# Kernel optimization log

Hardware: AMD Instinct MI355X
Metric: run time of the kernel (lower is better)

The kernel has to match this reference:

```python
import jax, jax.numpy as jnp
import numpy as np

N_QUBITS = 12
DIM = 2 ** N_QUBITS
N_RES_LAYERS = 3
N_HEADS = 2
N_ATTN_LAYERS = 2
SEQ_LEN = 64
HORIZON = 4
BATCH = 8
N_PARAMS = N_QUBITS * 2 * N_ATTN_LAYERS  # 48
FEAT = N_QUBITS * N_HEADS  # 24

# ---- static (numpy) precomputed gate structures (little-endian, qiskit convention) ----
_idx = np.arange(DIM)

def _cx_perm(c, t):
    # CNOT: flip target bit where control bit is 1 -> index permutation
    return np.where(((_idx >> c) & 1) == 1, _idx ^ (1 << t), _idx)

def _cz_phase(a, b):
    return (1.0 - 2.0 * (((_idx >> a) & 1) * ((_idx >> b) & 1))).astype(np.float32)

CX_LADDER = [jnp.asarray(_cx_perm(i, i + 1)) for i in range(N_QUBITS - 1)]
CX_RING = jnp.asarray(_cx_perm(N_QUBITS - 1, 0))
CX_LONG = jnp.asarray(_cx_perm(0, N_QUBITS - 1))
_CZ = []
for _layer in range(N_RES_LAYERS):
    _ph = np.ones(DIM, np.float32)
    for _i in range(_layer % 2, N_QUBITS - 1, 2):
        _ph *= _cz_phase(_i, _i + 1)
    _CZ.append(jnp.asarray(_ph))
# Qiskit Pauli label 'I'*i + 'Z' + 'I'*(n-i-1) acts on qubit n-1-i (big-endian labels)
Z_SIGNS = jnp.asarray(np.stack([
    (1.0 - 2.0 * ((_idx >> (N_QUBITS - 1 - i)) & 1)).astype(np.float32)
    for i in range(N_QUBITS)]))  # (n, DIM)


def _apply_1q(state, gate, q):
    # state: (..., DIM); gate: (2,2) or (...,2,2) broadcastable against leading dims
    hi = DIM >> (q + 1)
    lo = 1 << q
    s = state.reshape(state.shape[:-1] + (hi, 2, lo))
    out = jnp.einsum('...ij,...hjl->...hil', gate, s)
    return out.reshape(state.shape)


def _ry(theta):
    c = jnp.cos(theta / 2)
    s = jnp.sin(theta / 2)
    g = jnp.stack([jnp.stack([c, -s], -1), jnp.stack([s, c], -1)], -2)
    return g.astype(jnp.complex64)


def _rz(phi):
    em = jnp.exp(-0.5j * phi)
    ep = jnp.exp(0.5j * phi)
    z = jnp.zeros_like(em)
    return jnp.stack([jnp.stack([em, z], -1), jnp.stack([z, ep], -1)], -2)


def _u3(t, p, l):
    ct = jnp.cos(t / 2).astype(jnp.complex64)
    st = jnp.sin(t / 2).astype(jnp.complex64)
    return jnp.stack([jnp.stack([ct, -jnp.exp(1j * l) * st]),
                      jnp.stack([jnp.exp(1j * p) * st, jnp.exp(1j * (p + l)) * ct])])


def _encode_reservoir(x, res_params):
    # x: (B,T) normalized scalars -> batched statevectors (B,T,DIM)
    B, T = x.shape
    # H^{\otimes n} |0...0> = uniform superposition
    state = jnp.full((B, T, DIM), 1.0 / np.sqrt(DIM), jnp.complex64)
    for i in range(N_QUBITS):
        state = _apply_1q(state, _ry(x * np.pi * (i + 1) / N_QUBITS), i)
        state = _apply_1q(state, _rz(x * np.pi / (i + 1)), i)
    for p in CX_LADDER:
        state = state[..., p]
    state = state[..., CX_RING]
    # fixed random reservoir
    for layer in range(N_RES_LAYERS):
        for i in range(N_QUBITS):
            g = _u3(res_params[layer, i, 0], res_params[layer, i, 1], res_params[layer, i, 2])
            state = _apply_1q(state, g, i)
        state = state * _CZ[layer]
        state = state[..., CX_LONG]  # n > 2
    return state


def _project(state, params):
    # projection circuit: per layer RY/RZ on each qubit then CNOT ladder; then <Z_i>
    for layer in range(N_ATTN_LAYERS):
        for i in range(N_QUBITS):
            k = (layer * N_QUBITS + i) * 2
            state = _apply_1q(state, _ry(params[k]), i)
            state = _apply_1q(state, _rz(params[k + 1]), i)
        for p in CX_LADDER:
            state = state[..., p]
    probs = state.real ** 2 + state.imag ** 2  # (B,T,DIM)
    return jnp.einsum('btd,qd->btq', probs, Z_SIGNS)  # (B,T,n)


def setup_inputs() -> dict:
    key = jax.random.key(0)
    ks = jax.random.split(key, 6)
    sequence = jax.random.uniform(ks[0], (BATCH, SEQ_LEN), jnp.float32)
    res_params = jax.random.uniform(ks[1], (N_RES_LAYERS, N_QUBITS, 3), jnp.float32,
                                    minval=0.0, maxval=2.0 * np.pi)
    head_params = jax.random.uniform(ks[2], (N_HEADS, 3, N_PARAMS), jnp.float32,
                                     minval=0.0, maxval=2.0 * np.pi)
    W1 = jax.random.normal(ks[3], (FEAT, 2 * FEAT), jnp.float32) / np.sqrt(FEAT)
    b1 = jnp.zeros((2 * FEAT,), jnp.float32)
    W2 = jax.random.normal(ks[4], (2 * FEAT, HORIZON), jnp.float32) / np.sqrt(2 * FEAT)
    b2 = jnp.zeros((HORIZON,), jnp.float32)
    return {'sequence': sequence, 'res_params': res_params, 'head_params': head_params,
            'W1': W1, 'b1': b1, 'W2': W2, 'b2': b2}


def reference(sequence, res_params, head_params, W1, b1, W2, b2):
    states = _encode_reservoir(sequence, res_params)  # (B,T,DIM)
    T = sequence.shape[1]
    mask = jnp.triu(jnp.full((T, T), -1e9, jnp.float32), k=1)
    outs = []
    for h in range(N_HEADS):
        Q = _project(states, head_params[h, 0])
        K = _project(states, head_params[h, 1])
        V = _project(states, head_params[h, 2])
        scores = jnp.einsum('btd,bsd->bts', Q, K) / np.sqrt(N_QUBITS) + mask
        attn = jax.nn.softmax(scores, axis=-1)
        outs.append(jnp.einsum('bts,bsd->btd', attn, V))
    feats = jnp.concatenate(outs, -1)  # (B,T,FEAT)
    last = feats[:, -1, :]
    hdn = jax.nn.gelu(last @ W1 + b1, approximate=False)  # torch GELU default = exact erf
    pred = hdn @ W2 + b2  # (B, HORIZON)
    return pred
```

## Files before the change

### kernel.cpp

```cpp
#include <hip/hip_runtime.h>
#include <hip/hip_bf16.h>


#define PADDED 4224

__device__ __forceinline__ int PD(int j) { return j + (j >> 5); }

__device__ __forceinline__ int mapIdx(int j, int mode) {
  if (mode == 1) { int k = j ^ ((j >> 11) & 1); return k ^ ((k & 0x7FF) << 1); }
  if (mode == 2) { return j ^ ((j & 1) << 11); }
  if (mode == 3) { return j ^ ((j & 0x7FF) << 1); }
  return j;
}

template <int L>
__device__ __forceinline__ int layoutIdx(int tid, int r) {
  if constexpr (L == 0) return (tid << 4) | r;
  else if constexpr (L == 1) return ((tid & 0xF0) << 4) | (r << 4) | (tid & 15);
  else return (r << 8) | tid;
}

template <int L>
__device__ __forceinline__ void ldsRead16(const float* sR, const float* sI, int tid, int mode,
                                          float ar[16], float ai[16]) {
#pragma unroll
  for (int r = 0; r < 16; ++r) {
    int j = layoutIdx<L>(tid, r);
    int a = PD(mapIdx(j, mode));
    ar[r] = sR[a]; ai[r] = sI[a];
  }
}

template <int L>
__device__ __forceinline__ void ldsWrite16(float* sR, float* sI, int tid,
                                           const float ar[16], const float ai[16], int czmask) {
#pragma unroll
  for (int r = 0; r < 16; ++r) {
    int j = layoutIdx<L>(tid, r);
    float vr = ar[r], vi = ai[r];
    if (czmask) {
      float sg = (__popc((j & (j >> 1)) & czmask) & 1) ? -1.0f : 1.0f;
      vr *= sg; vi *= sg;
    }
    int a = PD(j);
    sR[a] = vr; sI[a] = vi;
  }
}

__device__ __forceinline__ void applyU34(float ar[16], float ai[16], const float (*ut)[8]) {
#pragma unroll
  for (int b = 0; b < 4; ++b) {
    const float* u = ut[b];
    float u00r = u[0];
    float u01r = u[2], u01i = u[3];
    float u10r = u[4], u10i = u[5], u11r = u[6], u11i = u[7];
#pragma unroll
    for (int m = 0; m < 8; ++m) {
      int p0 = ((m >> b) << (b + 1)) | (m & ((1 << b) - 1));
      int p1 = p0 | (1 << b);
      float x0r = ar[p0], x0i = ai[p0], x1r = ar[p1], x1i = ai[p1];
      ar[p0] = u00r * x0r + u01r * x1r - u01i * x1i;
      ai[p0] = u00r * x0i + u01r * x1i + u01i * x1r;
      ar[p1] = u10r * x0r - u10i * x0i + u11r * x1r - u11i * x1i;
      ai[p1] = u10r * x0i + u10i * x0r + u11r * x1i + u11i * x1r;
    }
  }
}

__device__ __forceinline__ void applyRyRz4(float ar[16], float ai[16], const float4* gt) {
#pragma unroll
  for (int b = 0; b < 4; ++b) {
    float4 g = gt[b];
    float c = g.x, s = g.y, zr = g.z, zi = g.w;
#pragma unroll
    for (int m = 0; m < 8; ++m) {
      int p0 = ((m >> b) << (b + 1)) | (m & ((1 << b) - 1));
      int p1 = p0 | (1 << b);
      float x0r = ar[p0], x0i = ai[p0], x1r = ar[p1], x1i = ai[p1];
      float n0r = c * x0r - s * x1r;
      float n0i = c * x0i - s * x1i;
      float wr  = s * x0r + c * x1r;
      float wi  = s * x0i + c * x1i;
      ar[p0] = n0r;              ai[p0] = n0i;
      ar[p1] = wr * zr - wi * zi; ai[p1] = wr * zi + wi * zr;
    }
  }
}

template <int L>
__device__ __forceinline__ void encPass(float* sR, float* sI, int tid, int mode,
                                        const float (*ut)[8], int czmask) {
  float ar[16], ai[16];
  ldsRead16<L>(sR, sI, tid, mode, ar, ai);
  if (mode != 0) __syncthreads();
  applyU34(ar, ai, ut);
  ldsWrite16<L>(sR, sI, tid, ar, ai, czmask);
  __syncthreads();
}

template <int L>
__device__ __forceinline__ void projPass(float* sR, float* sI, int tid, int mode, const float4* gt) {
  float ar[16], ai[16];
  ldsRead16<L>(sR, sI, tid, mode, ar, ai);
  if (mode != 0) __syncthreads();
  applyRyRz4(ar, ai, gt);
  ldsWrite16<L>(sR, sI, tid, ar, ai, 0);
  __syncthreads();
}

__device__ __forceinline__ void projFinal(const float* sR, const float* sI, int tid,
                                          const float4* gt, float feat[12]) {
  float ar[16], ai[16];
#pragma unroll
  for (int r = 0; r < 16; ++r) {
    int a = PD((r << 8) | tid);
    ar[r] = sR[a]; ai[r] = sI[a];
  }
  applyRyRz4(ar, ai, gt);
  float sp = 0.f, f0 = 0.f, f1 = 0.f, f2 = 0.f, f3 = 0.f;
  int pt = __popc(tid) & 1;
#pragma unroll
  for (int r = 0; r < 16; ++r) {
    float p = ar[r] * ar[r] + ai[r] * ai[r];
    sp += p;
    int tr = r ^ (r << 1); tr ^= (tr << 2);
    f0 += ((pt ^ ((tr >> 3) & 1)) ? -p : p);
    f1 += ((pt ^ ((tr >> 2) & 1)) ? -p : p);
    f2 += ((pt ^ ((tr >> 1) & 1)) ? -p : p);
    f3 += ((pt ^ (tr & 1)) ? -p : p);
  }
  feat[0] = f0; feat[1] = f1; feat[2] = f2; feat[3] = f3;
  int tt = tid ^ (tid << 1); tt ^= (tt << 2); tt ^= (tt << 4);
#pragma unroll
  for (int q = 4; q < 12; ++q)
    feat[q] = ((tt >> (11 - q)) & 1) ? -sp : sp;
}

__device__ __forceinline__ float waveReduce(float v) {
#pragma unroll
  for (int off = 32; off; off >>= 1) v += __shfl_xor(v, off, 64);
  return v;
}


__device__ __forceinline__ void buildQtab(float4* qtab, int tid, float x) {
  const float PI = 3.14159265358979323846f;
  const float RS2 = 0.70710678118654752440f;
  if (tid < 12) {
    int i = tid;
    float th = x * PI * (float)(i + 1) / 12.0f;
    float ph = x * PI / (float)(i + 1);
    float s, c;  sincosf(0.5f * th, &s, &c);
    float zi, zr; sincosf(0.5f * ph, &zi, &zr);
    float k0 = (c - s) * RS2, k1 = (c + s) * RS2;
    qtab[i] = make_float4(k0 * zr, -k0 * zi, k1 * zr, k1 * zi);
  }
}

__device__ __forceinline__ void buildUtab(float (*utab)[8], int tid, const float* resp) {
  if (tid >= 64 && tid < 100) {
    int i = tid - 64;
    const float* rp = resp + i * 3;
    float st, ct;  sincosf(0.5f * rp[0], &st, &ct);
    float sp2, cp; sincosf(rp[1], &sp2, &cp);
    float sl, cl;  sincosf(rp[2], &sl, &cl);
    float spl, cpl; sincosf(rp[1] + rp[2], &spl, &cpl);
    float* u = utab[i];
    u[0] = ct;       u[1] = 0.0f;
    u[2] = -cl * st; u[3] = -sl * st;
    u[4] = cp * st;  u[5] = sp2 * st;
    u[6] = cpl * ct; u[7] = spl * ct;
  }
}

__device__ __forceinline__ void initProduct(float* sRe, float* sIm, int tid, const float4* qtab) {
  float pr, pi;
  {
    float4 g = qtab[4];
    int sb = tid & 1;
    pr = sb ? g.z : g.x; pi = sb ? g.w : g.y;
  }
#pragma unroll
  for (int q = 5; q < 12; ++q) {
    float4 g = qtab[q];
    int sb = (tid >> (q - 4)) & 1;
    float fr = sb ? g.z : g.x, fi = sb ? g.w : g.y;
    float nr = pr * fr - pi * fi;
    pi = pr * fi + pi * fr; pr = nr;
  }
  float4 g0 = qtab[0], g1 = qtab[1], g2 = qtab[2], g3 = qtab[3];
  float c01r[4], c01i[4], c23r[4], c23i[4];
#pragma unroll
  for (int i2 = 0; i2 < 4; ++i2) {
    float f0r = (i2 & 1) ? g0.z : g0.x, f0i = (i2 & 1) ? g0.w : g0.y;
    float f1r = (i2 & 2) ? g1.z : g1.x, f1i = (i2 & 2) ? g1.w : g1.y;
    c01r[i2] = f0r * f1r - f0i * f1i; c01i[i2] = f0r * f1i + f0i * f1r;
    float f2r = (i2 & 1) ? g2.z : g2.x, f2i = (i2 & 1) ? g2.w : g2.y;
    float f3r = (i2 & 2) ? g3.z : g3.x, f3i = (i2 & 2) ? g3.w : g3.y;
    c23r[i2] = f2r * f3r - f2i * f3i; c23i[i2] = f2r * f3i + f2i * f3r;
  }
#pragma unroll
  for (int r = 0; r < 16; ++r) {
    float lr = c01r[r & 3] * c23r[r >> 2] - c01i[r & 3] * c23i[r >> 2];
    float li = c01r[r & 3] * c23i[r >> 2] + c01i[r & 3] * c23r[r >> 2];
    int a = PD((tid << 4) | r);
    sRe[a] = pr * lr - pi * li;
    sIm[a] = pr * li + pi * lr;
  }
}

__device__ __forceinline__ void buildPtab(float4* ptab, int tid, const float* hp) {
  if (tid < 24) {
    int k = tid * 2;
    float s, c;  sincosf(0.5f * hp[k], &s, &c);
    float zi, zr; sincosf(hp[k + 1], &zi, &zr);
    ptab[tid] = make_float4(c, s, zr, zi);
  }
}


__global__ __launch_bounds__(256, 2) void enc_kernel(
    const float* __restrict__ seq, const float* __restrict__ resp,
    float* __restrict__ wsStates) {
  __shared__ float sRe[PADDED], sIm[PADDED];
  __shared__ float4 qtab[12];
  __shared__ float utab[36][8];

  const int tid = threadIdx.x;
  const int blk = blockIdx.x;
  const float x = seq[blk];

  buildQtab(qtab, tid, x);
  buildUtab(utab, tid, resp);
  __syncthreads();

  initProduct(sRe, sIm, tid, qtab);
  __syncthreads();

  encPass<0>(sRe, sIm, tid, 1, &utab[0], 0);
  encPass<1>(sRe, sIm, tid, 0, &utab[4], 0);
  encPass<2>(sRe, sIm, tid, 0, &utab[8], 0x555);
  encPass<0>(sRe, sIm, tid, 2, &utab[12], 0);
  encPass<1>(sRe, sIm, tid, 0, &utab[16], 0);
  encPass<2>(sRe, sIm, tid, 0, &utab[20], 0x2AA);
  encPass<0>(sRe, sIm, tid, 2, &utab[24], 0);
  encPass<1>(sRe, sIm, tid, 0, &utab[28], 0);

  {
    float ar[16], ai[16];
    ldsRead16<2>(sRe, sIm, tid, 0, ar, ai);
    applyU34(ar, ai, &utab[32]);
    float* gR = wsStates + (size_t)blk * 8192;
    float* gI = gR + 4096;
#pragma unroll
    for (int r = 0; r < 16; ++r) {
      int j = (r << 8) | tid;
      float sg = (__popc((j & (j >> 1)) & 0x555) & 1) ? -1.0f : 1.0f;
      int g = j ^ ((j & 1) << 11);
      gR[g] = sg * ar[r];
      gI[g] = sg * ai[r];
    }
  }
}

__global__ __launch_bounds__(256, 4) void proj_kernel(
    const float* __restrict__ wsStates, const float* __restrict__ hparams,
    float* __restrict__ featBase) {
  __shared__ float sRe[PADDED], sIm[PADDED];
  __shared__ float4 ptab[24];
  __shared__ float red[4][12];

  const int tid = threadIdx.x;
  const int bid = blockIdx.x;
  int h, which, s;
  if (bid < 2048) { s = bid >> 2; int pp = bid & 3; h = pp >> 1; which = 1 + (pp & 1); }
  else            { int i = bid - 2048; h = i & 1; s = (((i >> 1) << 6) | 63); which = 0; }
  const int b = s >> 6, t = s & 63;

  buildPtab(ptab, tid, hparams + (h * 3 + which) * 48);

  float ar[16], ai[16];
  const float4* pR = (const float4*)(wsStates + (size_t)s * 8192 + (tid << 4));
  const float4* pI = (const float4*)(wsStates + (size_t)s * 8192 + 4096 + (tid << 4));
#pragma unroll
  for (int k = 0; k < 4; ++k) {
    float4 vr = pR[k], vi = pI[k];
    ar[4 * k] = vr.x; ar[4 * k + 1] = vr.y; ar[4 * k + 2] = vr.z; ar[4 * k + 3] = vr.w;
    ai[4 * k] = vi.x; ai[4 * k + 1] = vi.y; ai[4 * k + 2] = vi.z; ai[4 * k + 3] = vi.w;
  }
  __syncthreads();

  applyRyRz4(ar, ai, &ptab[0]);
  ldsWrite16<0>(sRe, sIm, tid, ar, ai, 0);
  __syncthreads();

  projPass<1>(sRe, sIm, tid, 0, &ptab[4]);
  projPass<2>(sRe, sIm, tid, 0, &ptab[8]);
  projPass<0>(sRe, sIm, tid, 3, &ptab[12]);
  projPass<1>(sRe, sIm, tid, 0, &ptab[16]);

  float feat[12];
  projFinal(sRe, sIm, tid, &ptab[20], feat);
#pragma unroll
  for (int q = 0; q < 12; ++q) feat[q] = waveReduce(feat[q]);
  int wid = tid >> 6;
  if ((tid & 63) == 0) {
#pragma unroll
    for (int q = 0; q < 12; ++q) red[wid][q] = feat[q];
  }
  __syncthreads();
  if (tid < 12) {
    float v = red[0][tid] + red[1][tid] + red[2][tid] + red[3][tid];
    float* dst;
    if (which == 1)      dst = featBase + (((h << 3) + b) * 64 + t) * 12;
    else if (which == 2) dst = featBase + 12288 + (((h << 3) + b) * 64 + t) * 12;
    else                 dst = featBase + 24576 + ((h << 3) + b) * 12;
    dst[tid] = v;
  }
}


__global__ __launch_bounds__(256, 2) void qstates_mono(
    const float* __restrict__ seq, const float* __restrict__ resp,
    const float* __restrict__ hparams, float* __restrict__ featBase) {
  __shared__ float sRe[PADDED], sIm[PADDED];
  __shared__ float4 qtab[12];
  __shared__ float utab[36][8];
  __shared__ float4 ptab[24];
  __shared__ float red[4][12];

  const int tid = threadIdx.x;
  const int blk = blockIdx.x;
  const int b = blk >> 6;
  const int t = blk & 63;
  const float x = seq[blk];

  buildQtab(qtab, tid, x);
  buildUtab(utab, tid, resp);
  __syncthreads();
  initProduct(sRe, sIm, tid, qtab);
  __syncthreads();

  for (int l = 0; l < 3; ++l) {
    int czm = (l & 1) ? 0x2AA : 0x555;
    encPass<0>(sRe, sIm, tid, (l == 0) ? 1 : 2, &utab[l * 12], 0);
    encPass<1>(sRe, sIm, tid, 0, &utab[l * 12 + 4], 0);
    encPass<2>(sRe, sIm, tid, 0, &utab[l * 12 + 8], czm);
  }

  float encR[16], encI[16];
#pragma unroll
  for (int r = 0; r < 16; ++r) {
    int j = (tid << 4) | r;
    int a = PD(j ^ ((j & 1) << 11));
    encR[r] = sRe[a]; encI[r] = sIm[a];
  }

  const int nproj = (t == 63) ? 6 : 4;
  for (int pj = 0; pj < nproj; ++pj) {
    int h, which;
    if (pj < 4) { h = pj >> 1; which = (pj & 1) ? 2 : 1; }
    else        { h = pj - 4;  which = 0; }
    buildPtab(ptab, tid, hparams + (h * 3 + which) * 48);
    __syncthreads();

    float ar[16], ai[16];
#pragma unroll
    for (int r = 0; r < 16; ++r) { ar[r] = encR[r]; ai[r] = encI[r]; }
    applyRyRz4(ar, ai, &ptab[0]);
    ldsWrite16<0>(sRe, sIm, tid, ar, ai, 0);
    __syncthreads();
    projPass<1>(sRe, sIm, tid, 0, &ptab[4]);
    projPass<2>(sRe, sIm, tid, 0, &ptab[8]);
    projPass<0>(sRe, sIm, tid, 3, &ptab[12]);
    projPass<1>(sRe, sIm, tid, 0, &ptab[16]);

    float feat[12];
    projFinal(sRe, sIm, tid, &ptab[20], feat);
#pragma unroll
    for (int q = 0; q < 12; ++q) feat[q] = waveReduce(feat[q]);
    int wid = tid >> 6;
    if ((tid & 63) == 0) {
#pragma unroll
      for (int q = 0; q < 12; ++q) red[wid][q] = feat[q];
    }
    __syncthreads();
    if (tid < 12) {
      float v = red[0][tid] + red[1][tid] + red[2][tid] + red[3][tid];
      float* dst;
      if (which == 1)      dst = featBase + (((h << 3) + b) * 64 + t) * 12;
      else if (which == 2) dst = featBase + 12288 + (((h << 3) + b) * 64 + t) * 12;
      else                 dst = featBase + 24576 + ((h << 3) + b) * 12;
      dst[tid] = v;
    }
    __syncthreads();
  }
}


__global__ __launch_bounds__(64) void qhead_kernel(
    const float* __restrict__ featBase,
    const float* __restrict__ W1, const float* __restrict__ b1,
    const float* __restrict__ W2, const float* __restrict__ b2,
    float* __restrict__ out) {
  __shared__ float feats[24];
  __shared__ float hdn[48];
  const int b = blockIdx.x;
  const int lane = threadIdx.x;
  const float* Kf = featBase;
  const float* Vf = featBase + 12288;
  const float* Qf = featBase + 24576;
  for (int h = 0; h < 2; ++h) {
    const float* q  = Qf + ((h << 3) + b) * 12;
    const float* kr = Kf + ((((h << 3) + b) << 6) + lane) * 12;
    float dot = 0.f;
#pragma unroll
    for (int d = 0; d < 12; ++d) dot += q[d] * kr[d];
    dot *= 0.288675134594812882f;
    float mx = dot;
#pragma unroll
    for (int off = 32; off; off >>= 1) mx = fmaxf(mx, __shfl_xor(mx, off, 64));
    float e = expf(dot - mx);
    float se = e;
#pragma unroll
    for (int off = 32; off; off >>= 1) se += __shfl_xor(se, off, 64);
    float a = e / se;
    const float* vr = Vf + ((((h << 3) + b) << 6) + lane) * 12;
#pragma unroll
    for (int d = 0; d < 12; ++d) {
      float v = a * vr[d];
#pragma unroll
      for (int off = 32; off; off >>= 1) v += __shfl_xor(v, off, 64);
      if (lane == 0) feats[h * 12 + d] = v;
    }
  }
  __syncthreads();
  if (lane < 48) {
    float acc = b1[lane];
#pragma unroll
    for (int f = 0; f < 24; ++f) acc += feats[f] * W1[f * 48 + lane];
    hdn[lane] = 0.5f * acc * (1.0f + erff(acc * 0.70710678118654752440f));
  }
  __syncthreads();
  if (lane < 4) {
    float acc = b2[lane];
#pragma unroll
    for (int k = 0; k < 48; ++k) acc += hdn[k] * W2[k * 4 + lane];
    out[(b << 2) | lane] = acc;
  }
}

extern "C" void kernel_launch(void* const* d_in, const int* in_sizes, int n_in,
                              void* d_out, int out_size, void* d_ws, size_t ws_size,
                              hipStream_t stream) {
  const float* seq     = (const float*)d_in[0];
  const float* resp    = (const float*)d_in[1];
  const float* hparams = (const float*)d_in[2];
  const float* W1      = (const float*)d_in[3];
  const float* b1      = (const float*)d_in[4];
  const float* W2      = (const float*)d_in[5];
  const float* b2      = (const float*)d_in[6];
  float* out = (float*)d_out;
  float* ws  = (float*)d_ws;

  const size_t needSplit = ((size_t)512 * 8192 + 24768) * sizeof(float);
  if (ws_size >= needSplit) {
    float* wsStates = ws;
    float* featBase = ws + (size_t)512 * 8192;
    hipLaunchKernelGGL(enc_kernel, dim3(512), dim3(256), 0, stream, seq, resp, wsStates);
    hipLaunchKernelGGL(proj_kernel, dim3(2064), dim3(256), 0, stream, wsStates, hparams, featBase);
    hipLaunchKernelGGL(qhead_kernel, dim3(8), dim3(64), 0, stream, featBase, W1, b1, W2, b2, out);
  } else {
    hipLaunchKernelGGL(qstates_mono, dim3(512), dim3(256), 0, stream, seq, resp, hparams, ws);
    hipLaunchKernelGGL(qhead_kernel, dim3(8), dim3(64), 0, stream, ws, W1, b1, W2, b2, out);
  }
}
```

Measured before the change: 150.4 us.

## Halve projection LDS footprint with phased half-buffer transposes and register-side final reduction

The projection kernel now keeps only half of the statevector in LDS at a time. Each transpose is done in two phases, split by one thread-index bit, and an address mapping drops that bit. This halves shared memory per block and raises the launch-bounds occupancy target from 4 to 8 blocks per CU. The final pass and the Z-expectation computation are folded into register-side parity sums instead of a separate LDS-based projFinal. In exchange, each transpose needs extra __syncthreads barriers and runs in serialized half-phases.

```diff
diff --git a/kernel.cpp b/kernel.cpp
--- a/kernel.cpp
+++ b/kernel.cpp
@@ -3,8 +3,12 @@
 
 
 #define PADDED 4224
+#define HPAD   2112
+
+#define LDSFENCE asm volatile("s_waitcnt lgkmcnt(0)" ::: "memory")
 
 __device__ __forceinline__ int PD(int j) { return j + (j >> 5); }
+__device__ __forceinline__ int PH(int i) { return i + (i >> 5); }
 
 __device__ __forceinline__ int mapIdx(int j, int mode) {
   if (mode == 1) { int k = j ^ ((j >> 11) & 1); return k ^ ((k & 0x7FF) << 1); }
@@ -17,7 +21,14 @@
 __device__ __forceinline__ int layoutIdx(int tid, int r) {
   if constexpr (L == 0) return (tid << 4) | r;
   else if constexpr (L == 1) return ((tid & 0xF0) << 4) | (r << 4) | (tid & 15);
-  else return (r << 8) | tid;
+  else if constexpr (L == 2) return (r << 8) | tid;
+  else return ((tid & 15) << 8) | (tid & 0xF0) | r;
+}
+
+template <int B>
+__device__ __forceinline__ int dropbit(int j) {
+  constexpr int lo = (1 << B) - 1;
+  return (j & lo) | ((j >> 1) & ~lo);
 }
 
 template <int L>
@@ -44,6 +55,28 @@
     }
     int a = PD(j);
     sR[a] = vr; sI[a] = vi;
+  }
+}
+
+template <int L, int B>
+__device__ __forceinline__ void hWrite16(float* hR, float* hI, int tid,
+                                         const float ar[16], const float ai[16]) {
+#pragma unroll
+  for (int r = 0; r < 16; ++r) {
+    int j = layoutIdx<L>(tid, r);
+    int a = PH(dropbit<B>(j));
+    hR[a] = ar[r]; hI[a] = ai[r];
+  }
+}
+
+template <int L, int B, int MODE>
+__device__ __forceinline__ void hRead16(const float* hR, const float* hI, int tid,
+                                        float ar[16], float ai[16]) {
+#pragma unroll
+  for (int r = 0; r < 16; ++r) {
+    int j = mapIdx(layoutIdx<L>(tid, r), MODE);
+    int a = PH(dropbit<B>(j));
+    ar[r] = hR[a]; ai[r] = hI[a];
   }
 }
 
@@ -263,10 +296,10 @@
   }
 }
 
-__global__ __launch_bounds__(256, 4) void proj_kernel(
+__global__ __launch_bounds__(256, 8) void proj_split(
     const float* __restrict__ wsStates, const float* __restrict__ hparams,
     float* __restrict__ featBase) {
-  __shared__ float sRe[PADDED], sIm[PADDED];
+  __shared__ float hRe[HPAD], hIm[HPAD];
   __shared__ float4 ptab[24];
   __shared__ float red[4][12];
 
@@ -290,17 +323,89 @@
   }
   __syncthreads();
 
+  const int ph7 = (tid >> 7) & 1;
+  const int ph3 = (tid >> 3) & 1;
+  const int ph0 = tid & 1;
+
   applyRyRz4(ar, ai, &ptab[0]);
-  ldsWrite16<0>(sRe, sIm, tid, ar, ai, 0);
-  __syncthreads();
-
-  projPass<1>(sRe, sIm, tid, 0, &ptab[4]);
-  projPass<2>(sRe, sIm, tid, 0, &ptab[8]);
-  projPass<0>(sRe, sIm, tid, 3, &ptab[12]);
-  projPass<1>(sRe, sIm, tid, 0, &ptab[16]);
-
+
+  if (ph7 == 0) { hWrite16<0, 11>(hRe, hIm, tid, ar, ai); LDSFENCE; hRead16<1, 11, 0>(hRe, hIm, tid, ar, ai); }
+  __syncthreads();
+  if (ph7 == 1) { hWrite16<0, 11>(hRe, hIm, tid, ar, ai); LDSFENCE; hRead16<1, 11, 0>(hRe, hIm, tid, ar, ai); }
+
+  applyRyRz4(ar, ai, &ptab[4]);
+
+  __syncthreads();
+  if (ph3 == 0) hWrite16<1, 3>(hRe, hIm, tid, ar, ai);
+  __syncthreads();
+  if (ph3 == 0) hRead16<2, 3, 0>(hRe, hIm, tid, ar, ai);
+  __syncthreads();
+  if (ph3 == 1) hWrite16<1, 3>(hRe, hIm, tid, ar, ai);
+  __syncthreads();
+  if (ph3 == 1) hRead16<2, 3, 0>(hRe, hIm, tid, ar, ai);
+
+  applyRyRz4(ar, ai, &ptab[8]);
+
+  __syncthreads();
+  if (ph0 == 0) hWrite16<2, 0>(hRe, hIm, tid, ar, ai);
+  __syncthreads();
+  if (ph0 == 0) hRead16<1, 0, 3>(hRe, hIm, tid, ar, ai);
+  __syncthreads();
+  if (ph0 == 1) hWrite16<2, 0>(hRe, hIm, tid, ar, ai);
+  __syncthreads();
+  if (ph0 == 1) hRead16<1, 0, 3>(hRe, hIm, tid, ar, ai);
+
+  applyRyRz4(ar, ai, &ptab[16]);
+
+  __syncthreads();
+  if (ph3 == 0) hWrite16<1, 3>(hRe, hIm, tid, ar, ai);
+  __syncthreads();
+  if (ph3 == 0) hRead16<2, 3, 0>(hRe, hIm, tid, ar, ai);
+  __syncthreads();
+  if (ph3 == 1) hWrite16<1, 3>(hRe, hIm, tid, ar, ai);
+  __syncthreads();
+  if (ph3 == 1) hRead16<2, 3, 0>(hRe, hIm, tid, ar, ai);
+
+  applyRyRz4(ar, ai, &ptab[20]);
+
+  __syncthreads();
+  if (ph7 == 0) { hWrite16<2, 7>(hRe, hIm, tid, ar, ai); LDSFENCE; hRead16<3, 7, 0>(hRe, hIm, tid, ar, ai); }
+  __syncthreads();
+  if (ph7 == 1) { hWrite16<2, 7>(hRe, hIm, tid, ar, ai); LDSFENCE; hRead16<3, 7, 0>(hRe, hIm, tid, ar, ai); }
+
+  applyRyRz4(ar, ai, &ptab[12]);
+  float A = 0.f, B2 = 0.f, B1 = 0.f, B0 = 0.f;
+#pragma unroll
+  for (int r = 0; r < 16; ++r) {
+    float p = ar[r] * ar[r] + ai[r] * ai[r];
+    int tr = r ^ (r << 1); tr ^= (tr << 2);
+    A  += ((tr >> 3) & 1) ? -p : p;
+    B2 += ((tr >> 2) & 1) ? -p : p;
+    B1 += ((tr >> 1) & 1) ? -p : p;
+    B0 += ((tr & 1)      ) ? -p : p;
+  }
+  int t03p = __popc(tid & 0x0F) & 1;
+  int t47p = __popc(tid & 0xF0) & 1;
+  int u4   = (tid >> 4) & 1;
+  int u45  = u4 ^ ((tid >> 5) & 1);
+  int u456 = u45 ^ ((tid >> 6) & 1);
+  int v0   = tid & 1;
+  int v01  = v0 ^ ((tid >> 1) & 1);
+  int v012 = v01 ^ ((tid >> 2) & 1);
   float feat[12];
-  projFinal(sRe, sIm, tid, &ptab[20], feat);
+  feat[0]  = (t47p ^ t03p) ? -A : A;
+  feat[1]  = (t47p ^ v012) ? -A : A;
+  feat[2]  = (t47p ^ v01)  ? -A : A;
+  feat[3]  = (t47p ^ v0)   ? -A : A;
+  feat[4]  = t47p ? -A : A;
+  feat[5]  = u456 ? -A : A;
+  feat[6]  = u45  ? -A : A;
+  feat[7]  = u4   ? -A : A;
+  feat[8]  = A;
+  feat[9]  = B2;
+  feat[10] = B1;
+  feat[11] = B0;
+
 #pragma unroll
   for (int q = 0; q < 12; ++q) feat[q] = waveReduce(feat[q]);
   int wid = tid >> 6;
@@ -468,7 +573,7 @@
     float* wsStates = ws;
     float* featBase = ws + (size_t)512 * 8192;
     hipLaunchKernelGGL(enc_kernel, dim3(512), dim3(256), 0, stream, seq, resp, wsStates);
-    hipLaunchKernelGGL(proj_kernel, dim3(2064), dim3(256), 0, stream, wsStates, hparams, featBase);
+    hipLaunchKernelGGL(proj_split, dim3(2064), dim3(256), 0, stream, wsStates, hparams, featBase);
     hipLaunchKernelGGL(qhead_kernel, dim3(8), dim3(64), 0, stream, featBase, W1, b1, W2, b2, out);
   } else {
     hipLaunchKernelGGL(qstates_mono, dim3(512), dim3(256), 0, stream, seq, resp, hparams, ws);
```

Measured after the change: 236.0 us. +56.9%, slower.
